# Kernel tuning notes

Hardware: AMD Instinct MI355X
Metric: run time of the kernel (lower is better)

## Reference

```python
import jax, jax.numpy as jnp
import numpy as np

INPUT, HIDDEN = 15, 20

def setup_inputs() -> dict:
    key = jax.random.key(0)
    k1, k2, k3, k4, k5 = jax.random.split(key, 5)
    B, T = 4096, 512
    s = 1.0 / np.sqrt(HIDDEN)  # torch default uniform init bound
    feature = jax.random.normal(k1, (B, T, INPUT), dtype=jnp.float32)
    W_ih = jax.random.uniform(k2, (HIDDEN, INPUT), jnp.float32, -s, s)
    W_hh = jax.random.uniform(k3, (HIDDEN, HIDDEN), jnp.float32, -s, s)
    b_ih = jax.random.uniform(k4, (HIDDEN,), jnp.float32, -s, s)
    b_hh = jax.random.uniform(k5, (HIDDEN,), jnp.float32, -s, s)
    return {"feature": feature, "W_ih": W_ih, "W_hh": W_hh, "b_ih": b_ih, "b_hh": b_hh}

def reference(feature, W_ih, W_hh, b_ih, b_hh):
    # h_t = tanh(x_t @ W_ih^T + b_ih + h_{t-1} @ W_hh^T + b_hh)
    B, T, _ = feature.shape
    # precompute input projections for all timesteps: [T, B, H]
    xp = jnp.einsum('bti,hi->tbh', feature, W_ih) + (b_ih + b_hh)
    h0 = jnp.zeros((B, HIDDEN), dtype=feature.dtype)
    def step(h, x_t):
        h_new = jnp.tanh(x_t + h @ W_hh.T)
        return h_new, None
    hn, _ = jax.lax.scan(step, h0, xp)
    return hn  # [B, H] == hn.squeeze() for num_layers=1
```

## Files before the change

### kernel.cpp

```cpp
#include <hip/hip_runtime.h>
#include <cstddef>


typedef float f4 __attribute__((ext_vector_type(4)));
typedef float g4 __attribute__((ext_vector_type(4), aligned(4)));
typedef _Float16 h2 __attribute__((ext_vector_type(2)));
typedef _Float16 v4h __attribute__((ext_vector_type(4)));
typedef _Float16 v8h __attribute__((ext_vector_type(8)));
typedef __fp16 p2 __attribute__((ext_vector_type(2)));

#define TT 512
#define IN 15
#define HD 20
#define NB 16

__device__ __forceinline__ float fexp2(float x) {
#if __has_builtin(__builtin_amdgcn_exp2f)
  return __builtin_amdgcn_exp2f(x);
#else
  return exp2f(x);
#endif
}
__device__ __forceinline__ h2 pk2(float a, float b) {
  p2 r = __builtin_amdgcn_cvt_pkrtz(a, b);
  return __builtin_bit_cast(h2, r);
}
__device__ __forceinline__ v4h cat4(h2 a, h2 b) {
  return __builtin_shufflevector(a, b, 0, 1, 2, 3);
}
__device__ __forceinline__ v8h cat8(v4h a, v4h b) {
  return __builtin_shufflevector(a, b, 0, 1, 2, 3, 4, 5, 6, 7);
}

__global__ __launch_bounds__(64) void rnn_mfma(
    const float* __restrict__ feature, const float* __restrict__ W_ih,
    const float* __restrict__ W_hh, const float* __restrict__ b_ih,
    const float* __restrict__ b_hh, float* __restrict__ out, int B) {
  const int l = threadIdx.x;
  const int G = l >> 4;
  const int mf = l & 15;
  const int b0 = blockIdx.x * NB;

  const float K2 = 2.8853900817779268f;

  const int jP = 5 * (mf >> 2) + (mf & 3);
  const int jQ = 5 * (mf >> 2) + 4;

  v8h AhhP, AhhQ;
#pragma unroll
  for (int i = 0; i < 8; ++i) {
    const int k = 5 * G + i;
    const float wP = (i < 5) ? -2.f * K2 * W_hh[jP * HD + k] : 0.f;
    const float wQ = (i < 5) ? -2.f * K2 * W_hh[jQ * HD + k] : 0.f;
    AhhP[i] = (_Float16)wP;
    AhhQ[i] = (_Float16)wQ;
  }
  const int k0 = (G < 3) ? 4 * G : 11;
  v4h AihP, AihQ;
#pragma unroll
  for (int i = 0; i < 4; ++i) {
    const int k = k0 + i;
    const bool dup = (G == 2 && i == 3);
    AihP[i] = (_Float16)((k < IN && !dup) ? K2 * W_ih[jP * IN + k] : 0.f);
    AihQ[i] = (_Float16)((k < IN && !dup) ? K2 * W_ih[jQ * IN + k] : 0.f);
  }
  f4 biasP, biasQ;
#pragma unroll
  for (int r = 0; r < 4; ++r) {
    const int jp = 5 * G + r, jq = 5 * G + 4;
    float rsP = 0.f, rsQ = 0.f;
#pragma unroll
    for (int k = 0; k < HD; ++k) {
      rsP += W_hh[jp * HD + k];
      rsQ += W_hh[jq * HD + k];
    }
    biasP[r] = K2 * (b_ih[jp] + b_hh[jp] + rsP);
    biasQ[r] = K2 * (b_ih[jq] + b_hh[jq] + rsQ);
  }

  const int b = min(b0 + mf, B - 1);
  const float* xbase = feature + (size_t)b * TT * IN + k0;
  auto load_x = [&](int t) -> g4 {
    return *(const g4*)(xbase + (size_t)t * IN);
  };

  g4 XR[8];
#pragma unroll
  for (int s = 1; s <= 8; ++s) XR[s & 7] = load_x(s);

  g4 x0 = load_x(0);
  v4h X0 = cat4(pk2(x0.x, x0.y), pk2(x0.z, x0.w));
  f4 cxPc = __builtin_amdgcn_mfma_f32_16x16x16f16(AihP, X0, biasP, 0, 0, 0);
  f4 cxQc = __builtin_amdgcn_mfma_f32_16x16x16f16(AihQ, X0, biasQ, 0, 0, 0);

  v8h Bh;
#pragma unroll
  for (int i = 0; i < 8; ++i) Bh[i] = (_Float16)((i < 5) ? 0.5f : 0.f);

  float uP[4], uQ0 = 0.5f;
#pragma unroll
  for (int r = 0; r < 4; ++r) uP[r] = 0.5f;

  const h2 zero2 = {(_Float16)0.f, (_Float16)0.f};

  for (int t = 0; t < TT; t += 8) {
#pragma unroll
    for (int u = 0; u < 8; ++u) {
      f4 aP = __builtin_amdgcn_mfma_f32_16x16x32_f16(AhhP, Bh, cxPc, 0, 0, 0);
      f4 aQ = __builtin_amdgcn_mfma_f32_16x16x32_f16(AhhQ, Bh, cxQc, 0, 0, 0);
      const int s = (u + 1) & 7;
      g4 xr = XR[s];
      v4h Xn = cat4(pk2(xr.x, xr.y), pk2(xr.z, xr.w));
      cxPc = __builtin_amdgcn_mfma_f32_16x16x16f16(AihP, Xn, biasP, 0, 0, 0);
      cxQc = __builtin_amdgcn_mfma_f32_16x16x16f16(AihQ, Xn, biasQ, 0, 0, 0);
      const int tn = t + u + 9;
      XR[s] = load_x(tn < TT ? tn : TT - 1);
#pragma unroll
      for (int r = 0; r < 4; ++r)
        uP[r] = __builtin_amdgcn_rcpf(1.f + fexp2(aP[r]));
      uQ0 = __builtin_amdgcn_rcpf(1.f + fexp2(aQ[0]));
      Bh = cat8(cat4(pk2(uP[0], uP[1]), pk2(uP[2], uP[3])),
                cat4(pk2(uQ0, 0.f), zero2));
    }
  }

  const int batch = b0 + mf;
  if (batch < B) {
    float* orow = out + (size_t)batch * HD;
#pragma unroll
    for (int r = 0; r < 4; ++r) orow[5 * G + r] = 1.f - 2.f * uP[r];
    orow[5 * G + 4] = 1.f - 2.f * uQ0;
  }
}

extern "C" void kernel_launch(void* const* d_in, const int* in_sizes, int n_in,
                              void* d_out, int out_size, void* d_ws, size_t ws_size,
                              hipStream_t stream) {
  const float* feature = (const float*)d_in[0];
  const float* W_ih    = (const float*)d_in[1];
  const float* W_hh    = (const float*)d_in[2];
  const float* b_ih    = (const float*)d_in[3];
  const float* b_hh    = (const float*)d_in[4];
  float* out = (float*)d_out;
  const int B = in_sizes[0] / (TT * IN);
  const int grid = (B + NB - 1) / NB;
  rnn_mfma<<<grid, 64, 0, stream>>>(feature, W_ih, W_hh, b_ih, b_hh, out, B);
}
```

Baseline: 209.7 us.

## Interleave two independent batch groups per wavefront to hide recurrence latency

Each 64-lane block now processes 32 batch rows as two independent 16-row recurrences, A and B. Their MFMA and transcendental chains are interleaved so one chain's latency can overlap the other's work. The loop is also software-pipelined so the hidden-state MFMA for the next step is issued before the activation. This halves the grid size and raises register use, which may reduce occupancy. The input prefetch depth shrinks from 8 to 4 steps per chain.

```diff
diff --git a/kernel.cpp b/kernel.cpp
--- a/kernel.cpp
+++ b/kernel.cpp
@@ -12,7 +12,7 @@
 #define TT 512
 #define IN 15
 #define HD 20
-#define NB 16
+#define NB 32
 
 __device__ __forceinline__ float fexp2(float x) {
 #if __has_builtin(__builtin_amdgcn_exp2f)
@@ -78,58 +78,102 @@
     biasQ[r] = K2 * (b_ih[jq] + b_hh[jq] + rsQ);
   }
 
-  const int b = min(b0 + mf, B - 1);
-  const float* xbase = feature + (size_t)b * TT * IN + k0;
-  auto load_x = [&](int t) -> g4 {
-    return *(const g4*)(xbase + (size_t)t * IN);
-  };
+  const int bA = min(b0 + mf, B - 1);
+  const int bB = min(b0 + 16 + mf, B - 1);
+  const float* xbA = feature + (size_t)bA * TT * IN + k0;
+  const float* xbB = feature + (size_t)bB * TT * IN + k0;
+  auto ldA = [&](int t) -> g4 { return *(const g4*)(xbA + (size_t)t * IN); };
+  auto ldB = [&](int t) -> g4 { return *(const g4*)(xbB + (size_t)t * IN); };
 
-  g4 XR[8];
+  g4 XRA[4], XRB[4];
 #pragma unroll
-  for (int s = 1; s <= 8; ++s) XR[s & 7] = load_x(s);
+  for (int t = 2; t <= 5; ++t) {
+    XRA[t & 3] = ldA(t);
+    XRB[t & 3] = ldB(t);
+  }
 
-  g4 x0 = load_x(0);
-  v4h X0 = cat4(pk2(x0.x, x0.y), pk2(x0.z, x0.w));
-  f4 cxPc = __builtin_amdgcn_mfma_f32_16x16x16f16(AihP, X0, biasP, 0, 0, 0);
-  f4 cxQc = __builtin_amdgcn_mfma_f32_16x16x16f16(AihQ, X0, biasQ, 0, 0, 0);
+  g4 xa0 = ldA(0), xb0 = ldB(0);
+  v4h XA = cat4(pk2(xa0.x, xa0.y), pk2(xa0.z, xa0.w));
+  v4h XB = cat4(pk2(xb0.x, xb0.y), pk2(xb0.z, xb0.w));
+  f4 cxAP = __builtin_amdgcn_mfma_f32_16x16x16f16(AihP, XA, biasP, 0, 0, 0);
+  f4 cxAQ = __builtin_amdgcn_mfma_f32_16x16x16f16(AihQ, XA, biasQ, 0, 0, 0);
+  f4 cxBP = __builtin_amdgcn_mfma_f32_16x16x16f16(AihP, XB, biasP, 0, 0, 0);
+  f4 cxBQ = __builtin_amdgcn_mfma_f32_16x16x16f16(AihQ, XB, biasQ, 0, 0, 0);
 
-  v8h Bh;
+  v8h BhA, BhB;
 #pragma unroll
-  for (int i = 0; i < 8; ++i) Bh[i] = (_Float16)((i < 5) ? 0.5f : 0.f);
+  for (int i = 0; i < 8; ++i) {
+    BhA[i] = (_Float16)((i < 5) ? 0.5f : 0.f);
+    BhB[i] = (_Float16)((i < 5) ? 0.5f : 0.f);
+  }
 
-  float uP[4], uQ0 = 0.5f;
-#pragma unroll
-  for (int r = 0; r < 4; ++r) uP[r] = 0.5f;
+  f4 aAP = __builtin_amdgcn_mfma_f32_16x16x32_f16(AhhP, BhA, cxAP, 0, 0, 0);
+  f4 aAQ = __builtin_amdgcn_mfma_f32_16x16x32_f16(AhhQ, BhA, cxAQ, 0, 0, 0);
+  f4 aBP = __builtin_amdgcn_mfma_f32_16x16x32_f16(AhhP, BhB, cxBP, 0, 0, 0);
+  f4 aBQ = __builtin_amdgcn_mfma_f32_16x16x32_f16(AhhQ, BhB, cxBQ, 0, 0, 0);
 
+  g4 xa1 = ldA(1), xb1 = ldB(1);
+  XA = cat4(pk2(xa1.x, xa1.y), pk2(xa1.z, xa1.w));
+  XB = cat4(pk2(xb1.x, xb1.y), pk2(xb1.z, xb1.w));
+  cxAP = __builtin_amdgcn_mfma_f32_16x16x16f16(AihP, XA, biasP, 0, 0, 0);
+  cxAQ = __builtin_amdgcn_mfma_f32_16x16x16f16(AihQ, XA, biasQ, 0, 0, 0);
+  cxBP = __builtin_amdgcn_mfma_f32_16x16x16f16(AihP, XB, biasP, 0, 0, 0);
+  cxBQ = __builtin_amdgcn_mfma_f32_16x16x16f16(AihQ, XB, biasQ, 0, 0, 0);
+
+  float uPA[4], uPB[4], uQA = 0.5f, uQB = 0.5f;
   const h2 zero2 = {(_Float16)0.f, (_Float16)0.f};
 
-  for (int t = 0; t < TT; t += 8) {
+#pragma unroll 8
+  for (int r = 1; r <= TT; ++r) {
+    uQA = __builtin_amdgcn_rcpf(1.f + fexp2(aAQ[0]));
 #pragma unroll
-    for (int u = 0; u < 8; ++u) {
-      f4 aP = __builtin_amdgcn_mfma_f32_16x16x32_f16(AhhP, Bh, cxPc, 0, 0, 0);
-      f4 aQ = __builtin_amdgcn_mfma_f32_16x16x32_f16(AhhQ, Bh, cxQc, 0, 0, 0);
-      const int s = (u + 1) & 7;
-      g4 xr = XR[s];
+    for (int q = 0; q < 4; ++q)
+      uPA[q] = __builtin_amdgcn_rcpf(1.f + fexp2(aAP[q]));
+    BhA = cat8(cat4(pk2(uPA[0], uPA[1]), pk2(uPA[2], uPA[3])),
+               cat4(pk2(uQA, 0.f), zero2));
+    aAP = __builtin_amdgcn_mfma_f32_16x16x32_f16(AhhP, BhA, cxAP, 0, 0, 0);
+    aAQ = __builtin_amdgcn_mfma_f32_16x16x32_f16(AhhQ, BhA, cxAQ, 0, 0, 0);
+    {
+      const int s = (r + 1) & 3;
+      g4 xr = XRA[s];
       v4h Xn = cat4(pk2(xr.x, xr.y), pk2(xr.z, xr.w));
-      cxPc = __builtin_amdgcn_mfma_f32_16x16x16f16(AihP, Xn, biasP, 0, 0, 0);
-      cxQc = __builtin_amdgcn_mfma_f32_16x16x16f16(AihQ, Xn, biasQ, 0, 0, 0);
-      const int tn = t + u + 9;
-      XR[s] = load_x(tn < TT ? tn : TT - 1);
+      cxAP = __builtin_amdgcn_mfma_f32_16x16x16f16(AihP, Xn, biasP, 0, 0, 0);
+      cxAQ = __builtin_amdgcn_mfma_f32_16x16x16f16(AihQ, Xn, biasQ, 0, 0, 0);
+      const int tn = r + 5;
+      XRA[s] = ldA(tn < TT ? tn : TT - 1);
+    }
+    uQB = __builtin_amdgcn_rcpf(1.f + fexp2(aBQ[0]));
 #pragma unroll
-      for (int r = 0; r < 4; ++r)
-        uP[r] = __builtin_amdgcn_rcpf(1.f + fexp2(aP[r]));
-      uQ0 = __builtin_amdgcn_rcpf(1.f + fexp2(aQ[0]));
-      Bh = cat8(cat4(pk2(uP[0], uP[1]), pk2(uP[2], uP[3])),
-                cat4(pk2(uQ0, 0.f), zero2));
+    for (int q = 0; q < 4; ++q)
+      uPB[q] = __builtin_amdgcn_rcpf(1.f + fexp2(aBP[q]));
+    BhB = cat8(cat4(pk2(uPB[0], uPB[1]), pk2(uPB[2], uPB[3])),
+               cat4(pk2(uQB, 0.f), zero2));
+    aBP = __builtin_amdgcn_mfma_f32_16x16x32_f16(AhhP, BhB, cxBP, 0, 0, 0);
+    aBQ = __builtin_amdgcn_mfma_f32_16x16x32_f16(AhhQ, BhB, cxBQ, 0, 0, 0);
+    {
+      const int s = (r + 1) & 3;
+      g4 xr = XRB[s];
+      v4h Xn = cat4(pk2(xr.x, xr.y), pk2(xr.z, xr.w));
+      cxBP = __builtin_amdgcn_mfma_f32_16x16x16f16(AihP, Xn, biasP, 0, 0, 0);
+      cxBQ = __builtin_amdgcn_mfma_f32_16x16x16f16(AihQ, Xn, biasQ, 0, 0, 0);
+      const int tn = r + 5;
+      XRB[s] = ldB(tn < TT ? tn : TT - 1);
     }
   }
 
-  const int batch = b0 + mf;
-  if (batch < B) {
-    float* orow = out + (size_t)batch * HD;
+  const int batchA = b0 + mf;
+  if (batchA < B) {
+    float* orow = out + (size_t)batchA * HD;
 #pragma unroll
-    for (int r = 0; r < 4; ++r) orow[5 * G + r] = 1.f - 2.f * uP[r];
-    orow[5 * G + 4] = 1.f - 2.f * uQ0;
+    for (int r = 0; r < 4; ++r) orow[5 * G + r] = 1.f - 2.f * uPA[r];
+    orow[5 * G + 4] = 1.f - 2.f * uQA;
+  }
+  const int batchB = b0 + 16 + mf;
+  if (batchB < B) {
+    float* orow = out + (size_t)batchB * HD;
+#pragma unroll
+    for (int r = 0; r < 4; ++r) orow[5 * G + r] = 1.f - 2.f * uPB[r];
+    orow[5 * G + 4] = 1.f - 2.f * uQB;
   }
 }
 
```

Result: slower. 285.8 us (+36.3%).
